# Kernel tuning notes

Measured on AMD Instinct MI355X. Metric: run time of the kernel, lower is better.

Reference implementation:

```python
import jax, jax.numpy as jnp
import numpy as np

B, N, C, OUT = 8, 2048, 128, 128

def setup_inputs() -> dict:
    key = jax.random.key(0)
    k1, k2, k3, k4, k5, k6 = jax.random.split(key, 6)
    x = jax.random.normal(k1, (B, N, C), dtype=jnp.float32)
    adj = jax.random.randint(k2, (B, N, N), 0, 2, dtype=jnp.int32)
    # fc: Linear(2*C, 1) + Sigmoid  (per-edge attention on concat(x_j, x_k))
    W_fc = jax.random.normal(k3, (2 * C, 1), dtype=jnp.float32) / np.sqrt(2 * C)
    b_fc = jax.random.normal(k4, (1,), dtype=jnp.float32) * 0.01
    # linear: Linear(C, OUT)
    W_lin = jax.random.normal(k5, (C, OUT), dtype=jnp.float32) / np.sqrt(C)
    b_lin = jax.random.normal(k6, (OUT,), dtype=jnp.float32) * 0.01
    return {"x": x, "adj": adj, "W_fc": W_fc, "b_fc": b_fc, "W_lin": W_lin, "b_lin": b_lin}

def reference(x, adj, W_fc, b_fc, W_lin, b_lin):
    # mode == 'global'
    # a_jk = sigmoid(W_fc . concat(x_j, x_k) + b_fc) where adj[j,k]==1, else 0.
    # Split the concat linear: score = (x_j . w1) + (x_k . w2) + b.
    Cdim = x.shape[-1]
    w1, w2 = W_fc[:Cdim, 0], W_fc[Cdim:, 0]
    sj = jnp.einsum('bnc,c->bn', x, w1)  # contribution of source node j
    sk = jnp.einsum('bnc,c->bn', x, w2)  # contribution of neighbor k
    scores = jax.nn.sigmoid(sj[:, :, None] + sk[:, None, :] + b_fc[0])  # [B,N,N]
    w = jnp.where(adj == 1, scores, jnp.float32(0))
    # row-normalize (divide each row by its sum)
    w = w / jnp.sum(w, axis=-1, keepdims=True)
    support = jnp.einsum('bjk,bkc->bjc', w, x)   # weighted aggregate
    return support @ W_lin + b_lin              # output projection
```

## Files before the change

kernel.cpp:

```cpp
#include <hip/hip_runtime.h>
#include <stdint.h>

#define BB 8
#define NN 2048
#define CC 128
#define OO 128

typedef __attribute__((ext_vector_type(8))) short bf16x8;
typedef __attribute__((ext_vector_type(4))) float f32x4;
typedef __attribute__((ext_vector_type(4))) int i32x4;
typedef __attribute__((ext_vector_type(4))) unsigned short u16x4;
typedef unsigned int u32;
typedef unsigned short u16;

__device__ __forceinline__ u16 f2bf(float f) {
    union { float f; u32 u; } v; v.f = f;
    u32 r = v.u + 0x7FFFu + ((v.u >> 16) & 1u);
    return (u16)(r >> 16);
}

__device__ __forceinline__ void gl_lds16(const u16* g, u16* l) {
    __builtin_amdgcn_global_load_lds(
        (__attribute__((address_space(1))) void*)(uintptr_t)g,
        (__attribute__((address_space(3))) void*)l, 16, 0, 0);
}

__global__ __launch_bounds__(256) void wt_kernel(
    const float* __restrict__ W_lin, u16* __restrict__ Wt)
{
    __shared__ float ws2[8][132];
    const int t = threadIdx.x, o0 = blockIdx.x * 8;
    f32x4 v = *(const f32x4*)(W_lin + (t >> 1) * OO + o0 + (t & 1) * 4);
    #pragma unroll
    for (int e = 0; e < 4; ++e) ws2[(t & 1) * 4 + e][t >> 1] = v[e];
    __syncthreads();
    const int oo = t >> 5, c0 = (t & 31) * 4;
    f32x4 u = *(const f32x4*)&ws2[oo][c0];
    u16x4 h;
    #pragma unroll
    for (int e = 0; e < 4; ++e) h[e] = f2bf(u[e]);
    *(u16x4*)(Wt + (size_t)(o0 + oo) * CC + c0) = h;
}

__global__ __launch_bounds__(256) void precompute_kernel(
    const float* __restrict__ x, const float* __restrict__ W_fc,
    const float* __restrict__ b_fc, const u16* __restrict__ Wt,
    float* __restrict__ sj, float* __restrict__ sk, u16* __restrict__ Yt)
{
    const int t = threadIdx.x, l = t & 63, w = t >> 6;
    const int sl = l & 15, g = l >> 4;
    const int b  = blockIdx.x >> 6;
    const int k0 = (blockIdx.x & 63) << 5;
    const int mt = w & 1, nb = (w >> 1) << 2;
    const int row = k0 + mt * 16 + sl;
    const float* xr = x + ((size_t)(b * NN + row) << 7);

    bf16x8 a[4];
    float p1 = 0.f, p2 = 0.f;
    #pragma unroll
    for (int ks = 0; ks < 4; ++ks) {
        f32x4 lo4 = *(const f32x4*)(xr + ks * 32 + g * 8);
        f32x4 hi4 = *(const f32x4*)(xr + ks * 32 + g * 8 + 4);
        f32x4 w1l = *(const f32x4*)(W_fc + ks * 32 + g * 8);
        f32x4 w1h = *(const f32x4*)(W_fc + ks * 32 + g * 8 + 4);
        f32x4 w2l = *(const f32x4*)(W_fc + CC + ks * 32 + g * 8);
        f32x4 w2h = *(const f32x4*)(W_fc + CC + ks * 32 + g * 8 + 4);
        bf16x8 av;
        #pragma unroll
        for (int e = 0; e < 4; ++e) {
            p1 += lo4[e] * w1l[e] + hi4[e] * w1h[e];
            p2 += lo4[e] * w2l[e] + hi4[e] * w2h[e];
            av[e]     = (short)f2bf(lo4[e]);
            av[e + 4] = (short)f2bf(hi4[e]);
        }
        a[ks] = av;
    }
    p1 += __shfl_xor(p1, 16); p1 += __shfl_xor(p1, 32);
    p2 += __shfl_xor(p2, 16); p2 += __shfl_xor(p2, 32);
    if (w < 2 && g == 0) {
        sj[b * NN + row] = p1 + b_fc[0];
        sk[b * NN + row] = p2;
    }

    f32x4 acc[4];
    #pragma unroll
    for (int i = 0; i < 4; ++i) acc[i] = (f32x4){0.f, 0.f, 0.f, 0.f};
    #pragma unroll
    for (int i = 0; i < 4; ++i) {
        const u16* wp = Wt + (size_t)((nb + i) * 16 + sl) * CC;
        #pragma unroll
        for (int ks = 0; ks < 4; ++ks) {
            bf16x8 bv = *(const bf16x8*)(wp + ks * 32 + g * 8);
            acc[i] = __builtin_amdgcn_mfma_f32_16x16x32_bf16(a[ks], bv, acc[i], 0, 0, 0);
        }
    }
    #pragma unroll
    for (int i = 0; i < 4; ++i) {
        const int o = (nb + i) * 16 + sl;
        u16x4 h;
        #pragma unroll
        for (int e = 0; e < 4; ++e) h[e] = f2bf(acc[i][e]);
        *(u16x4*)(Yt + (size_t)(b * OO + o) * NN + k0 + mt * 16 + g * 4) = h;
    }
}

__global__ __launch_bounds__(256, 2) void graphconv_main(
    const int* __restrict__ adj, const float* __restrict__ sj,
    const float* __restrict__ sk, const u16* __restrict__ Yt,
    const float* __restrict__ b_lin, float* __restrict__ out)
{
    __shared__ __align__(16) u16 ybuf[2][16384];
    __shared__ __align__(16) u16 pbuf[4096];
    __shared__ float Sld[32];

    const int t  = threadIdx.x;
    const int l  = t & 63, w = t >> 6;
    const int sw = l & 15, kg = l >> 4;
    const int lo = l & 31, hi = l >> 5;
    const int b  = blockIdx.x & 7;
    const int j0 = (blockIdx.x >> 3) << 5;

    const int* arow[4];
    float sjr[4];
    #pragma unroll
    for (int q = 0; q < 4; ++q) {
        const int R = j0 + w * 8 + 2 * q + hi;
        arow[q] = adj + ((size_t)b * NN + R) * NN + lo * 4;
        sjr[q]  = sj[b * NN + R];
    }
    const float* skp = sk + b * NN + lo * 4;

    u32 yoff[8];
    #pragma unroll
    for (int i = 0; i < 8; ++i) {
        int u  = (w * 8 + i) * 64 + l;
        int o  = u >> 4;
        int kc = (u & 15) ^ (o & 15);
        yoff[i] = (u32)(b * OO + o) * NN + kc * 8;
    }

    f32x4 acc[2][2];
    #pragma unroll
    for (int js = 0; js < 2; ++js)
        #pragma unroll
        for (int os = 0; os < 2; ++os) acc[js][os] = (f32x4){0.f, 0.f, 0.f, 0.f};
    float psum[4] = {0.f, 0.f, 0.f, 0.f};

    #pragma unroll
    for (int i = 0; i < 8; ++i)
        gl_lds16(Yt + yoff[i], &ybuf[0][(w * 8 + i) * 512]);
    i32x4 a_cur[4], a_n1[4];
    f32x4 s_cur, s_n1;
    #pragma unroll
    for (int q = 0; q < 4; ++q) a_cur[q] = *(const i32x4*)(arow[q]);
    s_cur = *(const f32x4*)(skp);
    #pragma unroll
    for (int q = 0; q < 4; ++q) a_n1[q] = *(const i32x4*)(arow[q] + 128);
    s_n1 = *(const f32x4*)(skp + 128);

    for (int kt = 0; kt < 16; ++kt) {
        const int cur = kt & 1;
        const int kt1 = (kt < 15) ? kt + 1 : 15;
        const int kt2 = (kt < 14) ? kt + 2 : 15;
        #pragma unroll
        for (int i = 0; i < 8; ++i)
            gl_lds16(Yt + yoff[i] + (kt1 << 7), &ybuf[cur ^ 1][(w * 8 + i) * 512]);
        i32x4 a_n2[4]; f32x4 s_n2;
        #pragma unroll
        for (int q = 0; q < 4; ++q) a_n2[q] = *(const i32x4*)(arow[q] + kt2 * 128);
        s_n2 = *(const f32x4*)(skp + kt2 * 128);

        u16x4 hq[4];
        #pragma unroll
        for (int q = 0; q < 4; ++q) {
            #pragma unroll
            for (int e = 0; e < 4; ++e) {
                float z  = sjr[q] + s_cur[e];
                float sg = __builtin_amdgcn_rcpf(1.0f + __expf(-z));
                float pv = a_cur[q][e] ? sg : 0.0f;
                psum[q] += pv;
                hq[q][e] = f2bf(pv);
            }
        }
        {
            const int kc = lo >> 1, hh = lo & 1;
            #pragma unroll
            for (int q = 0; q < 4; ++q) {
                const int R = w * 8 + 2 * q + hi;
                const int u = R * 16 + (kc ^ (R & 15));
                *(u16x4*)&pbuf[u * 8 + hh * 4] = hq[q];
            }
        }

        asm volatile("s_waitcnt vmcnt(18)" ::: "memory");
        asm volatile("s_waitcnt lgkmcnt(0)" ::: "memory");
        __builtin_amdgcn_s_barrier();
        asm volatile("" ::: "memory");

        #pragma unroll
        for (int kk = 0; kk < 4; ++kk) {
            const int kc = kk * 4 + kg;
            bf16x8 af[2], bfr[2];
            #pragma unroll
            for (int js = 0; js < 2; ++js)
                af[js] = *(const bf16x8*)&pbuf[((js * 16 + sw) * 16 + (kc ^ sw)) * 8];
            #pragma unroll
            for (int os = 0; os < 2; ++os) {
                int o = w * 32 + os * 16 + sw;
                bfr[os] = *(const bf16x8*)&ybuf[cur][(o * 16 + (kc ^ sw)) * 8];
            }
            #pragma unroll
            for (int js = 0; js < 2; ++js)
                #pragma unroll
                for (int os = 0; os < 2; ++os)
                    acc[js][os] = __builtin_amdgcn_mfma_f32_16x16x32_bf16(
                        af[js], bfr[os], acc[js][os], 0, 0, 0);
        }

        asm volatile("" ::: "memory");
        __builtin_amdgcn_s_barrier();
        asm volatile("" ::: "memory");

        #pragma unroll
        for (int q = 0; q < 4; ++q) a_cur[q] = a_n1[q];
        s_cur = s_n1;
        #pragma unroll
        for (int q = 0; q < 4; ++q) a_n1[q] = a_n2[q];
        s_n1 = s_n2;
    }

    #pragma unroll
    for (int q = 0; q < 4; ++q) {
        float s = psum[q];
        s += __shfl_xor(s, 1); s += __shfl_xor(s, 2); s += __shfl_xor(s, 4);
        s += __shfl_xor(s, 8); s += __shfl_xor(s, 16);
        if (lo == 0) Sld[w * 8 + 2 * q + hi] = s;
    }
    __syncthreads();

    #pragma unroll
    for (int js = 0; js < 2; ++js) {
        float rinv[4];
        #pragma unroll
        for (int i = 0; i < 4; ++i) rinv[i] = 1.0f / Sld[js * 16 + kg * 4 + i];
        #pragma unroll
        for (int os = 0; os < 2; ++os) {
            const int col = w * 32 + os * 16 + sw;
            const float bl = b_lin[col];
            #pragma unroll
            for (int i = 0; i < 4; ++i) {
                size_t row = (size_t)(b * NN + j0 + js * 16 + kg * 4 + i);
                out[row * OO + col] = acc[js][os][i] * rinv[i] + bl;
            }
        }
    }
}

extern "C" void kernel_launch(void* const* d_in, const int* in_sizes, int n_in,
                              void* d_out, int out_size, void* d_ws, size_t ws_size,
                              hipStream_t stream) {
    const float* x     = (const float*)d_in[0];
    const int*   adj   = (const int*)d_in[1];
    const float* W_fc  = (const float*)d_in[2];
    const float* b_fc  = (const float*)d_in[3];
    const float* W_lin = (const float*)d_in[4];
    const float* b_lin = (const float*)d_in[5];
    float* out = (float*)d_out;

    u16*   Yt = (u16*)d_ws;
    float* sj = (float*)((char*)d_ws + (size_t)BB * OO * NN * sizeof(u16));
    float* sk = sj + BB * NN;
    u16*   Wt = (u16*)(sk + BB * NN);

    wt_kernel<<<16, 256, 0, stream>>>(W_lin, Wt);
    precompute_kernel<<<512, 256, 0, stream>>>(x, W_fc, b_fc, Wt, sj, sk, Yt);
    graphconv_main<<<512, 256, 0, stream>>>(adj, sj, sk, Yt, b_lin, out);
}
```

Baseline: 50.77 us.

## Compute attention weights per 256-wide window and stage through LDS in two halves

Each wave now loads 8 full adjacency rows with 64 lanes covering 256 columns per window, instead of 4 row-pairs over 128 columns. The sigmoid weights for a window are computed once, then written to the shared P buffer in two halves (lanes 0-31 first, lanes 32-63 after the first MFMA step), feeding two 128-wide MFMA steps with double-buffered Y tiles. The intent is wider, more coalesced adjacency loads and fewer loop iterations of the score computation per MFMA step. The cost is more registers per thread (8 rows of prefetched adj in two buffers) and a hand-tuned waitcnt schedule that must stay correct.

```diff
diff --git a/kernel.cpp b/kernel.cpp
--- a/kernel.cpp
+++ b/kernel.cpp
@@ -116,27 +116,24 @@
     const int t  = threadIdx.x;
     const int l  = t & 63, w = t >> 6;
     const int sw = l & 15, kg = l >> 4;
-    const int lo = l & 31, hi = l >> 5;
+    const int kc = (l & 31) >> 1, hh = l & 1, ph = l >> 5;
     const int b  = blockIdx.x & 7;
     const int j0 = (blockIdx.x >> 3) << 5;
 
-    const int* arow[4];
-    float sjr[4];
-    #pragma unroll
-    for (int q = 0; q < 4; ++q) {
-        const int R = j0 + w * 8 + 2 * q + hi;
-        arow[q] = adj + ((size_t)b * NN + R) * NN + lo * 4;
-        sjr[q]  = sj[b * NN + R];
-    }
-    const float* skp = sk + b * NN + lo * 4;
+    const int* adjw = adj + ((size_t)b * NN + j0 + w * 8) * NN + l * 4;
+    const float* skw = sk + b * NN + l * 4;
+
+    float sjr[8];
+    #pragma unroll
+    for (int r = 0; r < 8; ++r) sjr[r] = sj[b * NN + j0 + w * 8 + r];
 
     u32 yoff[8];
     #pragma unroll
     for (int i = 0; i < 8; ++i) {
         int u  = (w * 8 + i) * 64 + l;
         int o  = u >> 4;
-        int kc = (u & 15) ^ (o & 15);
-        yoff[i] = (u32)(b * OO + o) * NN + kc * 8;
+        int c  = (u & 15) ^ (o & 15);
+        yoff[i] = (u32)(b * OO + o) * NN + c * 8;
     }
 
     f32x4 acc[2][2];
@@ -144,97 +141,127 @@
     for (int js = 0; js < 2; ++js)
         #pragma unroll
         for (int os = 0; os < 2; ++os) acc[js][os] = (f32x4){0.f, 0.f, 0.f, 0.f};
-    float psum[4] = {0.f, 0.f, 0.f, 0.f};
-
+    float psum[8];
+    #pragma unroll
+    for (int r = 0; r < 8; ++r) psum[r] = 0.f;
+
+    i32x4 aA[8], aB[8]; f32x4 sA, sB;
+    #pragma unroll
+    for (int r = 0; r < 8; ++r) aA[r] = *(const i32x4*)(adjw + (size_t)r * NN);
+    sA = *(const f32x4*)(skw);
+    #pragma unroll
+    for (int r = 0; r < 8; ++r) aB[r] = *(const i32x4*)(adjw + (size_t)r * NN + 256);
+    sB = *(const f32x4*)(skw + 256);
     #pragma unroll
     for (int i = 0; i < 8; ++i)
         gl_lds16(Yt + yoff[i], &ybuf[0][(w * 8 + i) * 512]);
-    i32x4 a_cur[4], a_n1[4];
-    f32x4 s_cur, s_n1;
-    #pragma unroll
-    for (int q = 0; q < 4; ++q) a_cur[q] = *(const i32x4*)(arow[q]);
-    s_cur = *(const f32x4*)(skp);
-    #pragma unroll
-    for (int q = 0; q < 4; ++q) a_n1[q] = *(const i32x4*)(arow[q] + 128);
-    s_n1 = *(const f32x4*)(skp + 128);
-
-    for (int kt = 0; kt < 16; ++kt) {
-        const int cur = kt & 1;
-        const int kt1 = (kt < 15) ? kt + 1 : 15;
-        const int kt2 = (kt < 14) ? kt + 2 : 15;
-        #pragma unroll
-        for (int i = 0; i < 8; ++i)
-            gl_lds16(Yt + yoff[i] + (kt1 << 7), &ybuf[cur ^ 1][(w * 8 + i) * 512]);
-        i32x4 a_n2[4]; f32x4 s_n2;
-        #pragma unroll
-        for (int q = 0; q < 4; ++q) a_n2[q] = *(const i32x4*)(arow[q] + kt2 * 128);
-        s_n2 = *(const f32x4*)(skp + kt2 * 128);
-
-        u16x4 hq[4];
-        #pragma unroll
-        for (int q = 0; q < 4; ++q) {
-            #pragma unroll
-            for (int e = 0; e < 4; ++e) {
-                float z  = sjr[q] + s_cur[e];
-                float sg = __builtin_amdgcn_rcpf(1.0f + __expf(-z));
-                float pv = a_cur[q][e] ? sg : 0.0f;
-                psum[q] += pv;
-                hq[q][e] = f2bf(pv);
-            }
-        }
-        {
-            const int kc = lo >> 1, hh = lo & 1;
-            #pragma unroll
-            for (int q = 0; q < 4; ++q) {
-                const int R = w * 8 + 2 * q + hi;
-                const int u = R * 16 + (kc ^ (R & 15));
-                *(u16x4*)&pbuf[u * 8 + hh * 4] = hq[q];
-            }
-        }
-
-        asm volatile("s_waitcnt vmcnt(18)" ::: "memory");
-        asm volatile("s_waitcnt lgkmcnt(0)" ::: "memory");
-        __builtin_amdgcn_s_barrier();
-        asm volatile("" ::: "memory");
-
-        #pragma unroll
-        for (int kk = 0; kk < 4; ++kk) {
-            const int kc = kk * 4 + kg;
-            bf16x8 af[2], bfr[2];
-            #pragma unroll
-            for (int js = 0; js < 2; ++js)
-                af[js] = *(const bf16x8*)&pbuf[((js * 16 + sw) * 16 + (kc ^ sw)) * 8];
-            #pragma unroll
-            for (int os = 0; os < 2; ++os) {
-                int o = w * 32 + os * 16 + sw;
-                bfr[os] = *(const bf16x8*)&ybuf[cur][(o * 16 + (kc ^ sw)) * 8];
-            }
-            #pragma unroll
-            for (int js = 0; js < 2; ++js)
-                #pragma unroll
-                for (int os = 0; os < 2; ++os)
-                    acc[js][os] = __builtin_amdgcn_mfma_f32_16x16x32_bf16(
-                        af[js], bfr[os], acc[js][os], 0, 0, 0);
-        }
-
-        asm volatile("" ::: "memory");
-        __builtin_amdgcn_s_barrier();
-        asm volatile("" ::: "memory");
-
-        #pragma unroll
-        for (int q = 0; q < 4; ++q) a_cur[q] = a_n1[q];
-        s_cur = s_n1;
-        #pragma unroll
-        for (int q = 0; q < 4; ++q) a_n1[q] = a_n2[q];
-        s_n1 = s_n2;
-    }
-
-    #pragma unroll
-    for (int q = 0; q < 4; ++q) {
-        float s = psum[q];
-        s += __shfl_xor(s, 1); s += __shfl_xor(s, 2); s += __shfl_xor(s, 4);
-        s += __shfl_xor(s, 8); s += __shfl_xor(s, 16);
-        if (lo == 0) Sld[w * 8 + 2 * q + hi] = s;
+
+#define WINDOW_BODY(M_, AV, SKV)                                              \
+    {                                                                         \
+        const int m_  = (M_);                                                 \
+        const int kt1 = 2 * m_ + 1;                                           \
+                           \
+        u16x4 hv[8];                                                          \
+        _Pragma("unroll")                                                     \
+        for (int r = 0; r < 8; ++r) {                                         \
+            i32x4 av = AV[r];                                                 \
+            _Pragma("unroll")                                                 \
+            for (int e = 0; e < 4; ++e) {                                     \
+                float z  = sjr[r] + SKV[e];                                   \
+                float sg = __builtin_amdgcn_rcpf(1.0f + __expf(-z));          \
+                float pv = av[e] ? sg : 0.0f;                                 \
+                psum[r] += pv;                                                \
+                hv[r][e] = f2bf(pv);                                          \
+            }                                                                 \
+        }                                                                     \
+        if (ph == 0) {                                                        \
+            _Pragma("unroll")                                                 \
+            for (int r = 0; r < 8; ++r) {                                     \
+                int R = w * 8 + r;                                            \
+                int u = R * 16 + (kc ^ (R & 15));                             \
+                *(u16x4*)&pbuf[u * 8 + hh * 4] = hv[r];                       \
+            }                                                                 \
+        }                                                                     \
+                                           \
+        _Pragma("unroll")                                                     \
+        for (int i = 0; i < 8; ++i)                                           \
+            gl_lds16(Yt + yoff[i] + (kt1 << 7), &ybuf[1][(w * 8 + i) * 512]); \
+                         \
+        {                                                                     \
+            const int mm = (m_ + 2 > 7) ? 7 : m_ + 2;                         \
+            _Pragma("unroll")                                                 \
+            for (int r = 0; r < 8; ++r)                                       \
+                AV[r] = *(const i32x4*)(adjw + (size_t)r * NN + mm * 256);    \
+            SKV = *(const f32x4*)(skw + mm * 256);                            \
+        }                                                                     \
+        asm volatile("s_waitcnt vmcnt(17)" ::: "memory");                     \
+        asm volatile("s_waitcnt lgkmcnt(0)" ::: "memory");                    \
+        __builtin_amdgcn_s_barrier();                                         \
+        asm volatile("" ::: "memory");                                        \
+        MFMA_STEP(0)                                                          \
+        asm volatile("" ::: "memory");                                        \
+        __builtin_amdgcn_s_barrier();                                         \
+        asm volatile("" ::: "memory");                                        \
+        if (ph == 1) {                                                        \
+            _Pragma("unroll")                                                 \
+            for (int r = 0; r < 8; ++r) {                                     \
+                int R = w * 8 + r;                                            \
+                int u = R * 16 + (kc ^ (R & 15));                             \
+                *(u16x4*)&pbuf[u * 8 + hh * 4] = hv[r];                       \
+            }                                                                 \
+        }                                                                     \
+                                           \
+        {                                                                     \
+            const int tn = (2 * m_ + 2 > 15) ? 15 : 2 * m_ + 2;               \
+            _Pragma("unroll")                                                 \
+            for (int i = 0; i < 8; ++i)                                       \
+                gl_lds16(Yt + yoff[i] + (tn << 7),                            \
+                         &ybuf[0][(w * 8 + i) * 512]);                        \
+        }                                                                     \
+        asm volatile("s_waitcnt vmcnt(17)" ::: "memory");                     \
+        asm volatile("s_waitcnt lgkmcnt(0)" ::: "memory");                    \
+        __builtin_amdgcn_s_barrier();                                         \
+        asm volatile("" ::: "memory");                                        \
+        MFMA_STEP(1)                                                          \
+        asm volatile("" ::: "memory");                                        \
+        __builtin_amdgcn_s_barrier();                                         \
+        asm volatile("" ::: "memory");                                        \
+    }
+
+#define MFMA_STEP(BUF)                                                        \
+    _Pragma("unroll")                                                         \
+    for (int kk = 0; kk < 4; ++kk) {                                          \
+        const int c = kk * 4 + kg;                                            \
+        bf16x8 af[2], bfr[2];                                                 \
+        _Pragma("unroll")                                                     \
+        for (int js = 0; js < 2; ++js)                                        \
+            af[js] = *(const bf16x8*)&pbuf[((js * 16 + sw) * 16 + (c ^ sw)) * 8]; \
+        _Pragma("unroll")                                                     \
+        for (int os = 0; os < 2; ++os) {                                      \
+            int o = w * 32 + os * 16 + sw;                                    \
+            bfr[os] = *(const bf16x8*)&ybuf[BUF][(o * 16 + (c ^ sw)) * 8];    \
+        }                                                                     \
+        _Pragma("unroll")                                                     \
+        for (int js = 0; js < 2; ++js)                                        \
+            _Pragma("unroll")                                                 \
+            for (int os = 0; os < 2; ++os)                                    \
+                acc[js][os] = __builtin_amdgcn_mfma_f32_16x16x32_bf16(        \
+                    af[js], bfr[os], acc[js][os], 0, 0, 0);                   \
+    }
+
+    for (int mi = 0; mi < 4; ++mi) {
+        WINDOW_BODY(2 * mi,     aA, sA)
+        WINDOW_BODY(2 * mi + 1, aB, sB)
+    }
+#undef WINDOW_BODY
+#undef MFMA_STEP
+
+    #pragma unroll
+    for (int r = 0; r < 8; ++r) {
+        float s = psum[r];
+        s += __shfl_xor(s, 1);  s += __shfl_xor(s, 2);  s += __shfl_xor(s, 4);
+        s += __shfl_xor(s, 8);  s += __shfl_xor(s, 16); s += __shfl_xor(s, 32);
+        if (l == 0) Sld[w * 8 + r] = s;
     }
     __syncthreads();
 
```

New measurement: 63.74 us. 25.6% more time.

## Load Yt MFMA operands directly from global and double-buffer P tile in LDS

Applied to the files above, without the earlier changes.

Removes the LDS staging of the Yt tile (global_load_lds into ybuf). Each wave now reads its B fragments for the MFMAs straight from global/L2 into registers. The P tile becomes double-buffered, so computing next tile's sigmoid weights overlaps with the current MFMAs and one barrier per iteration is dropped. The thread-to-row mapping is also changed so each thread handles 16 consecutive adj columns of one row. This cuts LDS usage and synchronisation, but makes Yt reads uncoalesced per-fragment global loads whose latency is exposed.

```diff
diff --git a/kernel.cpp b/kernel.cpp
--- a/kernel.cpp
+++ b/kernel.cpp
@@ -17,12 +17,6 @@
     union { float f; u32 u; } v; v.f = f;
     u32 r = v.u + 0x7FFFu + ((v.u >> 16) & 1u);
     return (u16)(r >> 16);
-}
-
-__device__ __forceinline__ void gl_lds16(const u16* g, u16* l) {
-    __builtin_amdgcn_global_load_lds(
-        (__attribute__((address_space(1))) void*)(uintptr_t)g,
-        (__attribute__((address_space(3))) void*)l, 16, 0, 0);
 }
 
 __global__ __launch_bounds__(256) void wt_kernel(
@@ -109,132 +103,114 @@
     const float* __restrict__ sk, const u16* __restrict__ Yt,
     const float* __restrict__ b_lin, float* __restrict__ out)
 {
-    __shared__ __align__(16) u16 ybuf[2][16384];
-    __shared__ __align__(16) u16 pbuf[4096];
+    __shared__ __align__(16) u16 pbuf[2][4096];
     __shared__ float Sld[32];
 
     const int t  = threadIdx.x;
     const int l  = t & 63, w = t >> 6;
     const int sw = l & 15, kg = l >> 4;
-    const int lo = l & 31, hi = l >> 5;
     const int b  = blockIdx.x & 7;
-    const int j0 = (blockIdx.x >> 3) << 5;
-
-    const int* arow[4];
-    float sjr[4];
+    const int j0 = (int)(blockIdx.x >> 3) << 5;
+
+    const int r  = t >> 3;
+    const int ks = (t & 7) << 4;
+    const float sjr = sj[b * NN + j0 + r];
+    const int*   arow = adj + ((size_t)b * NN + j0 + r) * NN + ks;
+    const float* skp  = sk + b * NN + ks;
+
+    const u16* ybase0 = Yt + (size_t)(b * OO + w * 32 + sw) * NN + kg * 8;
+    const u16* ybase1 = Yt + (size_t)(b * OO + w * 32 + 16 + sw) * NN + kg * 8;
+
+    f32x4 acc00 = {0,0,0,0}, acc01 = {0,0,0,0};
+    f32x4 acc10 = {0,0,0,0}, acc11 = {0,0,0,0};
+    float psum = 0.f;
+
+    i32x4 aE[4], aO[4]; f32x4 sE[4], sO[4];
     #pragma unroll
     for (int q = 0; q < 4; ++q) {
-        const int R = j0 + w * 8 + 2 * q + hi;
-        arow[q] = adj + ((size_t)b * NN + R) * NN + lo * 4;
-        sjr[q]  = sj[b * NN + R];
-    }
-    const float* skp = sk + b * NN + lo * 4;
-
-    u32 yoff[8];
-    #pragma unroll
-    for (int i = 0; i < 8; ++i) {
-        int u  = (w * 8 + i) * 64 + l;
-        int o  = u >> 4;
-        int kc = (u & 15) ^ (o & 15);
-        yoff[i] = (u32)(b * OO + o) * NN + kc * 8;
-    }
-
-    f32x4 acc[2][2];
-    #pragma unroll
-    for (int js = 0; js < 2; ++js)
-        #pragma unroll
-        for (int os = 0; os < 2; ++os) acc[js][os] = (f32x4){0.f, 0.f, 0.f, 0.f};
-    float psum[4] = {0.f, 0.f, 0.f, 0.f};
-
-    #pragma unroll
-    for (int i = 0; i < 8; ++i)
-        gl_lds16(Yt + yoff[i], &ybuf[0][(w * 8 + i) * 512]);
-    i32x4 a_cur[4], a_n1[4];
-    f32x4 s_cur, s_n1;
-    #pragma unroll
-    for (int q = 0; q < 4; ++q) a_cur[q] = *(const i32x4*)(arow[q]);
-    s_cur = *(const f32x4*)(skp);
-    #pragma unroll
-    for (int q = 0; q < 4; ++q) a_n1[q] = *(const i32x4*)(arow[q] + 128);
-    s_n1 = *(const f32x4*)(skp + 128);
-
-    for (int kt = 0; kt < 16; ++kt) {
-        const int cur = kt & 1;
-        const int kt1 = (kt < 15) ? kt + 1 : 15;
-        const int kt2 = (kt < 14) ? kt + 2 : 15;
-        #pragma unroll
-        for (int i = 0; i < 8; ++i)
-            gl_lds16(Yt + yoff[i] + (kt1 << 7), &ybuf[cur ^ 1][(w * 8 + i) * 512]);
-        i32x4 a_n2[4]; f32x4 s_n2;
-        #pragma unroll
-        for (int q = 0; q < 4; ++q) a_n2[q] = *(const i32x4*)(arow[q] + kt2 * 128);
-        s_n2 = *(const f32x4*)(skp + kt2 * 128);
-
-        u16x4 hq[4];
-        #pragma unroll
-        for (int q = 0; q < 4; ++q) {
-            #pragma unroll
-            for (int e = 0; e < 4; ++e) {
-                float z  = sjr[q] + s_cur[e];
-                float sg = __builtin_amdgcn_rcpf(1.0f + __expf(-z));
-                float pv = a_cur[q][e] ? sg : 0.0f;
-                psum[q] += pv;
-                hq[q][e] = f2bf(pv);
-            }
-        }
-        {
-            const int kc = lo >> 1, hh = lo & 1;
-            #pragma unroll
-            for (int q = 0; q < 4; ++q) {
-                const int R = w * 8 + 2 * q + hi;
-                const int u = R * 16 + (kc ^ (R & 15));
-                *(u16x4*)&pbuf[u * 8 + hh * 4] = hq[q];
-            }
-        }
-
-        asm volatile("s_waitcnt vmcnt(18)" ::: "memory");
-        asm volatile("s_waitcnt lgkmcnt(0)" ::: "memory");
-        __builtin_amdgcn_s_barrier();
-        asm volatile("" ::: "memory");
-
-        #pragma unroll
-        for (int kk = 0; kk < 4; ++kk) {
-            const int kc = kk * 4 + kg;
-            bf16x8 af[2], bfr[2];
-            #pragma unroll
-            for (int js = 0; js < 2; ++js)
-                af[js] = *(const bf16x8*)&pbuf[((js * 16 + sw) * 16 + (kc ^ sw)) * 8];
-            #pragma unroll
-            for (int os = 0; os < 2; ++os) {
-                int o = w * 32 + os * 16 + sw;
-                bfr[os] = *(const bf16x8*)&ybuf[cur][(o * 16 + (kc ^ sw)) * 8];
-            }
-            #pragma unroll
-            for (int js = 0; js < 2; ++js)
-                #pragma unroll
-                for (int os = 0; os < 2; ++os)
-                    acc[js][os] = __builtin_amdgcn_mfma_f32_16x16x32_bf16(
-                        af[js], bfr[os], acc[js][os], 0, 0, 0);
-        }
-
-        asm volatile("" ::: "memory");
-        __builtin_amdgcn_s_barrier();
-        asm volatile("" ::: "memory");
-
-        #pragma unroll
-        for (int q = 0; q < 4; ++q) a_cur[q] = a_n1[q];
-        s_cur = s_n1;
-        #pragma unroll
-        for (int q = 0; q < 4; ++q) a_n1[q] = a_n2[q];
-        s_n1 = s_n2;
-    }
-
+        aE[q] = *(const i32x4*)(arow + q * 4);
+        sE[q] = *(const f32x4*)(skp + q * 4);
+    }
     #pragma unroll
     for (int q = 0; q < 4; ++q) {
-        float s = psum[q];
+        aO[q] = *(const i32x4*)(arow + 128 + q * 4);
+        sO[q] = *(const f32x4*)(skp + 128 + q * 4);
+    }
+
+#define PSTORE(AV, SV, PAR)                                                   \
+    {                                                                         \
+        bf16x8 hv0, hv1;                                                      \
+        _Pragma("unroll")                                                     \
+        for (int q = 0; q < 4; ++q) {                                         \
+            _Pragma("unroll")                                                 \
+            for (int e = 0; e < 4; ++e) {                                     \
+                float z  = sjr + SV[q][e];                                    \
+                float sg = __builtin_amdgcn_rcpf(1.0f + __expf(-z));          \
+                float pv = AV[q][e] ? sg : 0.0f;                              \
+                psum += pv;                                                   \
+                if (q < 2) hv0[q * 4 + e]       = (short)f2bf(pv);            \
+                else       hv1[(q - 2) * 4 + e] = (short)f2bf(pv);            \
+            }                                                                 \
+        }                                                                     \
+        const int kcA = (t & 7) * 2;                                          \
+        const int uA  = r * 16 + (kcA ^ (r & 15));                            \
+        const int uB  = r * 16 + ((kcA + 1) ^ (r & 15));                      \
+        *(bf16x8*)&pbuf[PAR][uA * 8] = hv0;                                   \
+        *(bf16x8*)&pbuf[PAR][uB * 8] = hv1;                                   \
+    }
+
+    PSTORE(aE, sE, 0)
+    asm volatile("s_waitcnt lgkmcnt(0)" ::: "memory");
+    __builtin_amdgcn_s_barrier();
+    asm volatile("" ::: "memory");
+
+#define BODY(KT, AV, SV, AN, SN)                                              \
+    {                                                                         \
+        const int kt_ = (KT);                                                 \
+                   \
+        bf16x8 bfr0[4], bfr1[4];                                              \
+        _Pragma("unroll")                                                     \
+        for (int kk = 0; kk < 4; ++kk) {                                      \
+            bfr0[kk] = *(const bf16x8*)(ybase0 + kt_ * 128 + kk * 32);        \
+            bfr1[kk] = *(const bf16x8*)(ybase1 + kt_ * 128 + kk * 32);        \
+        }                                                                     \
+                        \
+        if (kt_ < 15) PSTORE(AV, SV, ((kt_ + 1) & 1))                         \
+                          \
+        if (kt_ < 14) {                                                       \
+            _Pragma("unroll")                                                 \
+            for (int q = 0; q < 4; ++q) {                                     \
+                AN[q] = *(const i32x4*)(arow + (kt_ + 2) * 128 + q * 4);      \
+                SN[q] = *(const f32x4*)(skp  + (kt_ + 2) * 128 + q * 4);      \
+            }                                                                 \
+        }                                                                     \
+                              \
+        _Pragma("unroll")                                                     \
+        for (int kk = 0; kk < 4; ++kk) {                                      \
+            const int kc = kk * 4 + kg;                                       \
+            bf16x8 af0 = *(const bf16x8*)&pbuf[kt_ & 1][(sw * 16 + (kc ^ sw)) * 8];        \
+            bf16x8 af1 = *(const bf16x8*)&pbuf[kt_ & 1][((16 + sw) * 16 + (kc ^ sw)) * 8]; \
+            acc00 = __builtin_amdgcn_mfma_f32_16x16x32_bf16(af0, bfr0[kk], acc00, 0, 0, 0);\
+            acc01 = __builtin_amdgcn_mfma_f32_16x16x32_bf16(af0, bfr1[kk], acc01, 0, 0, 0);\
+            acc10 = __builtin_amdgcn_mfma_f32_16x16x32_bf16(af1, bfr0[kk], acc10, 0, 0, 0);\
+            acc11 = __builtin_amdgcn_mfma_f32_16x16x32_bf16(af1, bfr1[kk], acc11, 0, 0, 0);\
+        }                                                                     \
+        asm volatile("s_waitcnt lgkmcnt(0)" ::: "memory");                    \
+        __builtin_amdgcn_s_barrier();                                         \
+        asm volatile("" ::: "memory");                                        \
+    }
+
+    for (int m = 0; m < 8; ++m) {
+        BODY(2 * m,     aO, sO, aE, sE)
+        BODY(2 * m + 1, aE, sE, aO, sO)
+    }
+#undef BODY
+#undef PSTORE
+
+    {
+        float s = psum;
         s += __shfl_xor(s, 1); s += __shfl_xor(s, 2); s += __shfl_xor(s, 4);
-        s += __shfl_xor(s, 8); s += __shfl_xor(s, 16);
-        if (lo == 0) Sld[w * 8 + 2 * q + hi] = s;
+        if ((l & 7) == 0) Sld[r] = s;
     }
     __syncthreads();
 
@@ -243,14 +219,17 @@
         float rinv[4];
         #pragma unroll
         for (int i = 0; i < 4; ++i) rinv[i] = 1.0f / Sld[js * 16 + kg * 4 + i];
+        const f32x4 a0 = js ? acc10 : acc00;
+        const f32x4 a1 = js ? acc11 : acc01;
         #pragma unroll
         for (int os = 0; os < 2; ++os) {
             const int col = w * 32 + os * 16 + sw;
             const float bl = b_lin[col];
+            const f32x4 av = os ? a1 : a0;
             #pragma unroll
             for (int i = 0; i < 4; ++i) {
                 size_t row = (size_t)(b * NN + j0 + js * 16 + kg * 4 + i);
-                out[row * OO + col] = acc[js][os][i] * rinv[i] + bl;
+                out[row * OO + col] = av[i] * rinv[i] + bl;
             }
         }
     }
```

Measured after the change: 65.06 us. 1.28x slower.

## Double-buffer probability tile and merge barriers to overlap sigmoid with MFMA

Applied to the files above, without the earlier changes.

Makes the probability LDS buffer double-buffered and software-pipelines the loop so the sigmoid tile for step t+1 is computed and stored while MFMAs consume tile t. This halves the barriers per iteration from two to one. It also unrolls the loop by two with ping-pong adjacency registers, removing the per-iteration register shuffles. The cost is extra LDS (8 KB more per block) and a more complex prologue and epilogue. The vmcnt accounting now depends on load ordering inside the macro.

```diff
diff --git a/kernel.cpp b/kernel.cpp
--- a/kernel.cpp
+++ b/kernel.cpp
@@ -110,7 +110,7 @@
     const float* __restrict__ b_lin, float* __restrict__ out)
 {
     __shared__ __align__(16) u16 ybuf[2][16384];
-    __shared__ __align__(16) u16 pbuf[4096];
+    __shared__ __align__(16) u16 pbuf[2][4096];
     __shared__ float Sld[32];
 
     const int t  = threadIdx.x;
@@ -146,87 +146,114 @@
         for (int os = 0; os < 2; ++os) acc[js][os] = (f32x4){0.f, 0.f, 0.f, 0.f};
     float psum[4] = {0.f, 0.f, 0.f, 0.f};
 
+#define SIGP(AV, SV, PAR)                                                     \
+    {                                                                         \
+        u16x4 hq[4];                                                          \
+        _Pragma("unroll")                                                     \
+        for (int q = 0; q < 4; ++q) {                                         \
+            _Pragma("unroll")                                                 \
+            for (int e = 0; e < 4; ++e) {                                     \
+                float z  = sjr[q] + SV[e];                                    \
+                float sg = __builtin_amdgcn_rcpf(1.0f + __expf(-z));          \
+                float pv = AV[q][e] ? sg : 0.0f;                              \
+                psum[q] += pv;                                                \
+                hq[q][e] = f2bf(pv);                                          \
+            }                                                                 \
+        }                                                                     \
+        const int kc_ = lo >> 1, hh_ = lo & 1;                                \
+        _Pragma("unroll")                                                     \
+        for (int q = 0; q < 4; ++q) {                                         \
+            const int R = w * 8 + 2 * q + hi;                                 \
+            const int u = R * 16 + (kc_ ^ (R & 15));                          \
+            *(u16x4*)&pbuf[PAR][u * 8 + hh_ * 4] = hq[q];                     \
+        }                                                                     \
+    }
+
     #pragma unroll
     for (int i = 0; i < 8; ++i)
         gl_lds16(Yt + yoff[i], &ybuf[0][(w * 8 + i) * 512]);
-    i32x4 a_cur[4], a_n1[4];
-    f32x4 s_cur, s_n1;
-    #pragma unroll
-    for (int q = 0; q < 4; ++q) a_cur[q] = *(const i32x4*)(arow[q]);
-    s_cur = *(const f32x4*)(skp);
-    #pragma unroll
-    for (int q = 0; q < 4; ++q) a_n1[q] = *(const i32x4*)(arow[q] + 128);
-    s_n1 = *(const f32x4*)(skp + 128);
-
-    for (int kt = 0; kt < 16; ++kt) {
-        const int cur = kt & 1;
-        const int kt1 = (kt < 15) ? kt + 1 : 15;
-        const int kt2 = (kt < 14) ? kt + 2 : 15;
-        #pragma unroll
-        for (int i = 0; i < 8; ++i)
-            gl_lds16(Yt + yoff[i] + (kt1 << 7), &ybuf[cur ^ 1][(w * 8 + i) * 512]);
-        i32x4 a_n2[4]; f32x4 s_n2;
-        #pragma unroll
-        for (int q = 0; q < 4; ++q) a_n2[q] = *(const i32x4*)(arow[q] + kt2 * 128);
-        s_n2 = *(const f32x4*)(skp + kt2 * 128);
-
-        u16x4 hq[4];
-        #pragma unroll
-        for (int q = 0; q < 4; ++q) {
+    i32x4 aT[4], aE[4], aO[4];
+    f32x4 sT, sE, sO;
+    #pragma unroll
+    for (int q = 0; q < 4; ++q) aT[q] = *(const i32x4*)(arow[q]);
+    sT = *(const f32x4*)(skp);
+    #pragma unroll
+    for (int q = 0; q < 4; ++q) aE[q] = *(const i32x4*)(arow[q] + 128);
+    sE = *(const f32x4*)(skp + 128);
+    #pragma unroll
+    for (int q = 0; q < 4; ++q) aO[q] = *(const i32x4*)(arow[q] + 256);
+    sO = *(const f32x4*)(skp + 256);
+    SIGP(aT, sT, 0)
+    asm volatile("s_waitcnt lgkmcnt(0)" ::: "memory");
+    __builtin_amdgcn_s_barrier();
+    asm volatile("" ::: "memory");
+
+#define TILE_BODY(T, AC, SC)                                                  \
+    {                                                                         \
+        const int T_ = (T);                                                   \
+        const int tn = T_ + 1;                                                \
+        const int tp = (T_ + 3 > 15) ? 15 : T_ + 3;                           \
+        const int pn = tn & 1, pc = T_ & 1;                                   \
+        _Pragma("unroll")                                                     \
+        for (int i = 0; i < 8; ++i)                                           \
+            gl_lds16(Yt + yoff[i] + (tn << 7), &ybuf[pn][(w * 8 + i) * 512]); \
+        SIGP(AC, SC, pn)                                                      \
+        _Pragma("unroll")                                                     \
+        for (int q = 0; q < 4; ++q)                                           \
+            AC[q] = *(const i32x4*)(arow[q] + tp * 128);                      \
+        SC = *(const f32x4*)(skp + tp * 128);                                 \
+        asm volatile("s_waitcnt vmcnt(18)" ::: "memory");                     \
+        _Pragma("unroll")                                                     \
+        for (int kk = 0; kk < 4; ++kk) {                                      \
+            const int kc = kk * 4 + kg;                                       \
+            bf16x8 af[2], bfr[2];                                             \
+            _Pragma("unroll")                                                 \
+            for (int js = 0; js < 2; ++js)                                    \
+                af[js] = *(const bf16x8*)&pbuf[pc][((js * 16 + sw) * 16 + (kc ^ sw)) * 8]; \
+            _Pragma("unroll")                                                 \
+            for (int os = 0; os < 2; ++os) {                                  \
+                int o = w * 32 + os * 16 + sw;                                \
+                bfr[os] = *(const bf16x8*)&ybuf[pc][(o * 16 + (kc ^ sw)) * 8]; \
+            }                                                                 \
+            _Pragma("unroll")                                                 \
+            for (int js = 0; js < 2; ++js)                                    \
+                _Pragma("unroll")                                             \
+                for (int os = 0; os < 2; ++os)                                \
+                    acc[js][os] = __builtin_amdgcn_mfma_f32_16x16x32_bf16(    \
+                        af[js], bfr[os], acc[js][os], 0, 0, 0);               \
+        }                                                                     \
+        asm volatile("s_waitcnt lgkmcnt(0)" ::: "memory");                    \
+        __builtin_amdgcn_s_barrier();                                         \
+        asm volatile("" ::: "memory");                                        \
+    }
+
+    for (int m = 0; m < 7; ++m) {
+        TILE_BODY(2 * m,     aE, sE)
+        TILE_BODY(2 * m + 1, aO, sO)
+    }
+    TILE_BODY(14, aE, sE)
+#undef TILE_BODY
+#undef SIGP
+
+    asm volatile("s_waitcnt vmcnt(0)" ::: "memory");
+    #pragma unroll
+    for (int kk = 0; kk < 4; ++kk) {
+        const int kc = kk * 4 + kg;
+        bf16x8 af[2], bfr[2];
+        #pragma unroll
+        for (int js = 0; js < 2; ++js)
+            af[js] = *(const bf16x8*)&pbuf[1][((js * 16 + sw) * 16 + (kc ^ sw)) * 8];
+        #pragma unroll
+        for (int os = 0; os < 2; ++os) {
+            int o = w * 32 + os * 16 + sw;
+            bfr[os] = *(const bf16x8*)&ybuf[1][(o * 16 + (kc ^ sw)) * 8];
+        }
+        #pragma unroll
+        for (int js = 0; js < 2; ++js)
             #pragma unroll
-            for (int e = 0; e < 4; ++e) {
-                float z  = sjr[q] + s_cur[e];
-                float sg = __builtin_amdgcn_rcpf(1.0f + __expf(-z));
-                float pv = a_cur[q][e] ? sg : 0.0f;
-                psum[q] += pv;
-                hq[q][e] = f2bf(pv);
-            }
-        }
-        {
-            const int kc = lo >> 1, hh = lo & 1;
-            #pragma unroll
-            for (int q = 0; q < 4; ++q) {
-                const int R = w * 8 + 2 * q + hi;
-                const int u = R * 16 + (kc ^ (R & 15));
-                *(u16x4*)&pbuf[u * 8 + hh * 4] = hq[q];
-            }
-        }
-
-        asm volatile("s_waitcnt vmcnt(18)" ::: "memory");
-        asm volatile("s_waitcnt lgkmcnt(0)" ::: "memory");
-        __builtin_amdgcn_s_barrier();
-        asm volatile("" ::: "memory");
-
-        #pragma unroll
-        for (int kk = 0; kk < 4; ++kk) {
-            const int kc = kk * 4 + kg;
-            bf16x8 af[2], bfr[2];
-            #pragma unroll
-            for (int js = 0; js < 2; ++js)
-                af[js] = *(const bf16x8*)&pbuf[((js * 16 + sw) * 16 + (kc ^ sw)) * 8];
-            #pragma unroll
-            for (int os = 0; os < 2; ++os) {
-                int o = w * 32 + os * 16 + sw;
-                bfr[os] = *(const bf16x8*)&ybuf[cur][(o * 16 + (kc ^ sw)) * 8];
-            }
-            #pragma unroll
-            for (int js = 0; js < 2; ++js)
-                #pragma unroll
-                for (int os = 0; os < 2; ++os)
-                    acc[js][os] = __builtin_amdgcn_mfma_f32_16x16x32_bf16(
-                        af[js], bfr[os], acc[js][os], 0, 0, 0);
-        }
-
-        asm volatile("" ::: "memory");
-        __builtin_amdgcn_s_barrier();
-        asm volatile("" ::: "memory");
-
-        #pragma unroll
-        for (int q = 0; q < 4; ++q) a_cur[q] = a_n1[q];
-        s_cur = s_n1;
-        #pragma unroll
-        for (int q = 0; q < 4; ++q) a_n1[q] = a_n2[q];
-        s_n1 = s_n2;
+            for (int os = 0; os < 2; ++os)
+                acc[js][os] = __builtin_amdgcn_mfma_f32_16x16x32_bf16(
+                    af[js], bfr[os], acc[js][os], 0, 0, 0);
     }
 
     #pragma unroll
```

Result: slower. 62.64 us (+23.4%).
